# Performance work log

Measured on AMD Instinct MI355X. Metric: run time of the kernel, lower is better.

Reference implementation:

```python
import jax, jax.numpy as jnp
import numpy as np

B, N, S = 64, 128, 100          # batch, pod_num, seq_len
E, H, M = 64, 128, 3            # embed_dim, hidden_dim, modal_num
VOCAB = 2000
FIN = M * S * (E + 1)           # shared_encoder in_features = 19500
FG = M * H                      # gat feature dim = 384
MAX_EVENT_LEN = 100.0
LEAKY_ALPHA = 0.2


def setup_inputs() -> dict:
    key = jax.random.key(0)
    ks = jax.random.split(key, 16)
    inp = {
        "l_e": jax.random.randint(ks[0], (B, N, S), 0, VOCAB),
        "m_e": jax.random.randint(ks[1], (B, N, S), 0, VOCAB),
        "t_e": jax.random.randint(ks[2], (B, N, S), 0, VOCAB),
        "l_c": jax.random.uniform(ks[3], (B, N, S), jnp.float32) * 100.0,
        "m_c": jax.random.uniform(ks[4], (B, N, S), jnp.float32) * 100.0,
        "t_c": jax.random.uniform(ks[5], (B, N, S), jnp.float32) * 100.0,
        "adj": (jax.random.uniform(ks[6], (N, N)) > 0.5).astype(jnp.float32),
        # learned parameters (weights stored as (in, out); y = x @ W + b)
        "emb": jax.random.normal(ks[7], (VOCAB, E), jnp.float32) * 0.02,
        "W_se": jax.random.normal(ks[8], (FIN, 3 * H), jnp.float32) * (1.0 / np.sqrt(FIN)),
        "b_se": jnp.zeros((3 * H,), jnp.float32),
        "gat_W": jax.random.normal(ks[9], (FG, FG), jnp.float32) * (1.0 / np.sqrt(FG)),
        "gat_a": jax.random.normal(ks[10], (2 * FG, 1), jnp.float32) * 0.1,
        "W1": jax.random.normal(ks[11], (FG * N, N), jnp.float32) * (1.0 / np.sqrt(FG * N)),
        "b1": jnp.zeros((N,), jnp.float32),
    }
    return inp


def gat_layer(x, adj, W, a):
    """Faithful GraphAttentionLayer (concat=True, dropout=0) without materializing
    the [B,N,N,2F] a_input: e_ij = leakyrelu(a1.h_i + a2.h_j)."""
    h = x @ W                                      # [B,N,F]
    F_ = W.shape[1]
    a1, a2 = a[:F_, 0], a[F_:, 0]
    e = jax.nn.leaky_relu(
        (h @ a1)[:, :, None] + (h @ a2)[:, None, :], LEAKY_ALPHA
    )                                              # [B,N,N]
    att = jnp.where(adj > 0, e, -1e12)
    att = jax.nn.softmax(att, axis=-1)
    return jax.nn.relu(att @ h)                    # [B,N,F]


def reference(l_e, m_e, t_e, l_c, m_c, t_c, adj, emb, W_se, b_se, gat_W, gat_a, W1, b1):
    # embedding lookup + concat normalized event counts -> [B,N,S,E+1] per modality
    log_r = jnp.concatenate([emb[l_e], (l_c / MAX_EVENT_LEN)[..., None]], -1)
    metric_r = jnp.concatenate([emb[m_e], (m_c / MAX_EVENT_LEN)[..., None]], -1)
    trace_r = jnp.concatenate([emb[t_e], (t_c / MAX_EVENT_LEN)[..., None]], -1)
    # shared encoder: cat on feature dim, flatten per node, dense -> [B,N,3H]
    fused = jnp.concatenate([log_r, metric_r, trace_r], -1).reshape(B, N, -1)
    fusion_r = fused @ W_se + b_se
    # GAT + residual + linear head (use_gat_linear path)
    out = gat_layer(fusion_r, adj, gat_W, gat_a)
    x = fusion_r + out
    x = x.reshape(B, -1) @ W1 + b1                 # [B,N]
    return (x, fusion_r)
```

## Files before the change

kernel.cpp:

```cpp
#include <hip/hip_runtime.h>

#define KB_TOT 305
#define KPAD   19520
#define BROW   39040

typedef __attribute__((ext_vector_type(8))) short bf16x8_t;
typedef __attribute__((ext_vector_type(4))) float f32x4_t;

typedef const __attribute__((address_space(1))) unsigned int GAS_u32;
typedef __attribute__((address_space(3))) unsigned int LAS_u32;

__device__ inline unsigned short f2bf(float x) {
    union { float f; unsigned u; } a; a.f = x;
    unsigned r = a.u + 0x7fffu + ((a.u >> 16) & 1u);
    return (unsigned short)(r >> 16);
}
__device__ inline float bf2f(unsigned short h) {
    union { unsigned u; float f; } a; a.u = ((unsigned)h) << 16; return a.f;
}
__device__ inline unsigned long long pack4bf(float x, float y, float z, float w) {
    return (unsigned long long)f2bf(x) | ((unsigned long long)f2bf(y) << 16)
         | ((unsigned long long)f2bf(z) << 32) | ((unsigned long long)f2bf(w) << 48);
}

__global__ __launch_bounds__(256) void emb_bf_kernel(const float* __restrict__ emb,
                                                     unsigned short* __restrict__ ebf) {
    int i4 = (blockIdx.x * 256 + threadIdx.x) * 4;
    float4 v = *(const float4*)(emb + i4);
    *(unsigned long long*)(ebf + i4) = pack4bf(v.x, v.y, v.z, v.w);
}

__global__ __launch_bounds__(256) void ac_bf_kernel(const float* __restrict__ l_c,
                                                    const float* __restrict__ m_c,
                                                    const float* __restrict__ t_c,
                                                    unsigned short* __restrict__ Ac) {
    int lin = blockIdx.x * 256 + threadIdx.x;
    int row = lin / 80, c4 = (lin - row * 80) * 4;
    float vv[4];
    #pragma unroll
    for (int ii = 0; ii < 4; ++ii) {
        int t = c4 + ii;
        float x = 0.f;
        if (t < 300) {
            int m = t / 100, s = t - m * 100;
            const float* C = (m == 0) ? l_c : ((m == 1) ? m_c : t_c);
            x = C[row * 100 + s] * 0.01f;
        }
        vv[ii] = x;
    }
    *(unsigned long long*)(Ac + row * 320 + c4) = pack4bf(vv[0], vv[1], vv[2], vv[3]);
}

__global__ __launch_bounds__(256) void build_B_kernel(const float* __restrict__ W_se,
                                                      unsigned short* __restrict__ Bws) {
    int kb = blockIdx.x;
    int h0 = blockIdx.y * 64;
    __shared__ float tl[64 * 68];
    int tid = threadIdx.x;
    int rr = tid >> 2, c16 = (tid & 3) * 16;
    float4 v[4];
    if (kb < 300) {
        int m = kb / 100, s = kb - m * 100;
        const float* srcp = W_se + (s * 195 + m * 65 + rr) * 384 + h0 + c16;
        #pragma unroll
        for (int ii = 0; ii < 4; ++ii) v[ii] = *(const float4*)(srcp + ii * 4);
    } else {
        int t = (kb - 300) * 64 + rr;
        if (t < 300) {
            int m = t / 100, s = t - m * 100;
            const float* srcp = W_se + (s * 195 + m * 65 + 64) * 384 + h0 + c16;
            #pragma unroll
            for (int ii = 0; ii < 4; ++ii) v[ii] = *(const float4*)(srcp + ii * 4);
        } else {
            #pragma unroll
            for (int ii = 0; ii < 4; ++ii) v[ii] = make_float4(0.f, 0.f, 0.f, 0.f);
        }
    }
    #pragma unroll
    for (int ii = 0; ii < 4; ++ii) *(float4*)(tl + rr * 68 + c16 + ii * 4) = v[ii];
    __syncthreads();
    int c = tid >> 2, r16 = (tid & 3) * 16;
    unsigned long long* dst8 =
        (unsigned long long*)(Bws + (unsigned)(h0 + c) * KPAD + kb * 64 + r16);
    #pragma unroll
    for (int q = 0; q < 4; ++q) {
        int rb = r16 + q * 4;
        dst8[q] = pack4bf(tl[(rb + 0) * 68 + c], tl[(rb + 1) * 68 + c],
                          tl[(rb + 2) * 68 + c], tl[(rb + 3) * 68 + c]);
    }
}

__global__ __launch_bounds__(256) void wt_bf_kernel(const float* __restrict__ W,
                                                    unsigned short* __restrict__ WT) {
    int k0 = blockIdx.x * 64, n0 = blockIdx.y * 64;
    __shared__ float tl[64 * 68];
    int tid = threadIdx.x;
    int rr = tid >> 2, c16 = (tid & 3) * 16;
    #pragma unroll
    for (int ii = 0; ii < 4; ++ii)
        *(float4*)(tl + rr * 68 + c16 + ii * 4) = *(const float4*)(W + (k0 + rr) * 384 + n0 + c16 + ii * 4);
    __syncthreads();
    int c = tid >> 2, r16 = (tid & 3) * 16;
    unsigned long long* dst8 = (unsigned long long*)(WT + (n0 + c) * 384 + k0 + r16);
    #pragma unroll
    for (int q = 0; q < 4; ++q) {
        int rb = r16 + q * 4;
        dst8[q] = pack4bf(tl[(rb + 0) * 68 + c], tl[(rb + 1) * 68 + c],
                          tl[(rb + 2) * 68 + c], tl[(rb + 3) * 68 + c]);
    }
}

__global__ __launch_bounds__(256) void gemm_fused_kernel(
    const int* __restrict__ l_e, const int* __restrict__ m_e, const int* __restrict__ t_e,
    const unsigned short* __restrict__ emb_bf, const unsigned short* __restrict__ Ac_bf,
    const unsigned short* __restrict__ Bws, float* __restrict__ fusion_d,
    float* __restrict__ P) {

    __shared__ alignas(16) unsigned short Al[128 * 64];
    __shared__ alignas(16) unsigned short Bl[128 * 64];

    const int tid  = threadIdx.x;
    const int lane = tid & 63;
    const int wid  = tid >> 6;

    int bid = blockIdx.x;
    int lin = (bid & 7) * 96 + (bid >> 3);
    const int mt = lin % 64;
    int rest = lin / 64;
    const int nt = rest % 3;
    const int kc = rest / 3;
    const int bm0 = mt * 128;
    const int h0  = nt * 128;
    int kb        = (kc == 0) ? 0 : (77 + (kc - 1) * 76);
    const int kbe = 77 + kc * 76 > KB_TOT ? KB_TOT : 77 + kc * 76;

    const int l7 = lane & 7, l3 = lane >> 3;
    const int voffA = ((l7 ^ l3) << 4);
    const int rowg0 = bm0 + wid * 32 + l3;

    f32x4_t acc[4][4];
    #pragma unroll
    for (int i = 0; i < 4; ++i)
        #pragma unroll
        for (int j = 0; j < 4; ++j) acc[i][j] = (f32x4_t){0.f, 0.f, 0.f, 0.f};

    const int wr = wid >> 1, wc = wid & 1;
    const int l15 = lane & 15, l4 = lane >> 4;

    int idx4[4];
    if (kb < 300) {
        int m = kb / 100, s = kb - m * 100;
        const int* I = (m == 0) ? l_e : ((m == 1) ? m_e : t_e);
        const int* Ib = I + rowg0 * 100 + s;
        idx4[0] = Ib[0]; idx4[1] = Ib[800]; idx4[2] = Ib[1600]; idx4[3] = Ib[2400];
    }

    for (; kb < kbe; ++kb) {
        if (kb < 300) {
            #pragma unroll
            for (int p = 0; p < 4; ++p) {
                const char* src = (const char*)emb_bf + ((long)idx4[p] << 7) + voffA;
                __builtin_amdgcn_global_load_lds((GAS_u32*)src,
                    (LAS_u32*)((char*)Al + (wid * 4 + p) * 1024), 16, 0, 0);
            }
        } else {
            int q = kb - 300;
            #pragma unroll
            for (int p = 0; p < 4; ++p) {
                const char* src = (const char*)Ac_bf + (long)(rowg0 + p * 8) * 640
                                + q * 128 + voffA;
                __builtin_amdgcn_global_load_lds((GAS_u32*)src,
                    (LAS_u32*)((char*)Al + (wid * 4 + p) * 1024), 16, 0, 0);
            }
        }
        #pragma unroll
        for (int p = 0; p < 4; ++p) {
            int ch = wid * 4 + p;
            int hl = ch * 8 + l3;
            long gb = (long)(h0 + hl) * BROW + kb * 128 + ((l7 << 4) ^ (l3 << 4));
            __builtin_amdgcn_global_load_lds((GAS_u32*)((const char*)Bws + gb),
                                             (LAS_u32*)((char*)Bl + ch * 1024), 16, 0, 0);
        }
        int kn = kb + 1;
        if (kn < 300 && kn < kbe) {
            int m = kn / 100, s = kn - m * 100;
            const int* I = (m == 0) ? l_e : ((m == 1) ? m_e : t_e);
            const int* Ib = I + rowg0 * 100 + s;
            idx4[0] = Ib[0]; idx4[1] = Ib[800]; idx4[2] = Ib[1600]; idx4[3] = Ib[2400];
        }
        __syncthreads();
        #pragma unroll
        for (int ks = 0; ks < 2; ++ks) {
            int kb2 = ks * 64 + l4 * 16;
            bf16x8_t af[4], bfr[4];
            #pragma unroll
            for (int i = 0; i < 4; ++i) {
                int row = wr * 64 + i * 16 + l15;
                af[i]  = *(const bf16x8_t*)((const char*)Al + row * 128 + (kb2 ^ ((row & 7) << 4)));
                int col = wc * 64 + i * 16 + l15;
                bfr[i] = *(const bf16x8_t*)((const char*)Bl + col * 128 + (kb2 ^ ((col & 7) << 4)));
            }
            #pragma unroll
            for (int i = 0; i < 4; ++i)
                #pragma unroll
                for (int j = 0; j < 4; ++j)
                    acc[i][j] = __builtin_amdgcn_mfma_f32_16x16x32_bf16(af[i], bfr[j], acc[i][j], 0, 0, 0);
        }
        __syncthreads();
    }
    float* dst = (kc == 0) ? fusion_d : (P + (size_t)(kc - 1) * 3145728);
    #pragma unroll
    for (int i = 0; i < 4; ++i)
        #pragma unroll
        for (int j = 0; j < 4; ++j)
            #pragma unroll
            for (int r = 0; r < 4; ++r) {
                int row = bm0 + wr * 64 + i * 16 + l4 * 4 + r;
                int col = h0 + wc * 64 + j * 16 + l15;
                dst[row * 384 + col] = acc[i][j][r];
            }
}

__global__ __launch_bounds__(256) void reduce_fusion_kernel(float* __restrict__ fusion_d,
                                                            const float* __restrict__ P,
                                                            const float* __restrict__ b_se,
                                                            unsigned short* __restrict__ fusion_bf) {
    int i4 = blockIdx.x * 256 + threadIdx.x;
    int col4 = (i4 % 96) * 4;
    float4 a = *(const float4*)(fusion_d + i4 * 4);
    float4 p0 = *(const float4*)(P + (size_t)i4 * 4);
    float4 p1 = *(const float4*)(P + 3145728 + (size_t)i4 * 4);
    float4 p2 = *(const float4*)(P + 6291456 + (size_t)i4 * 4);
    float4 bs = *(const float4*)(b_se + col4);
    float4 r;
    r.x = a.x + p0.x + p1.x + p2.x + bs.x;
    r.y = a.y + p0.y + p1.y + p2.y + bs.y;
    r.z = a.z + p0.z + p1.z + p2.z + bs.z;
    r.w = a.w + p0.w + p1.w + p2.w + bs.w;
    *(float4*)(fusion_d + i4 * 4) = r;
    *(unsigned long long*)(fusion_bf + i4 * 4) = pack4bf(r.x, r.y, r.z, r.w);
}

__global__ __launch_bounds__(256) void gat_h_kernel(const unsigned short* __restrict__ fusion_bf,
                                                    const unsigned short* __restrict__ WT,
                                                    unsigned short* __restrict__ hT) {
    __shared__ alignas(16) unsigned short Al[128 * 64];
    __shared__ alignas(16) unsigned short Bl[128 * 64];
    const int tid  = threadIdx.x;
    const int lane = tid & 63;
    const int wid  = tid >> 6;
    const int b  = blockIdx.x;
    const int c0 = blockIdx.y * 128;
    const int l7 = lane & 7, l3 = lane >> 3;
    const int voffA = ((l7 ^ l3) << 4);
    const int wr = wid >> 1, wc = wid & 1;
    const int l15 = lane & 15, l4 = lane >> 4;

    f32x4_t acc[4][4];
    #pragma unroll
    for (int i = 0; i < 4; ++i)
        #pragma unroll
        for (int j = 0; j < 4; ++j) acc[i][j] = (f32x4_t){0.f, 0.f, 0.f, 0.f};

    for (int kb = 0; kb < 6; ++kb) {
        #pragma unroll
        for (int p = 0; p < 4; ++p) {
            int ch = wid * 4 + p;
            int rl = ch * 8 + l3;
            long ga = (long)(b * 128 + rl) * 768 + kb * 128 + voffA;
            __builtin_amdgcn_global_load_lds((GAS_u32*)((const char*)fusion_bf + ga),
                                             (LAS_u32*)((char*)Al + ch * 1024), 16, 0, 0);
            long gb = (long)(c0 + rl) * 768 + kb * 128 + voffA;
            __builtin_amdgcn_global_load_lds((GAS_u32*)((const char*)WT + gb),
                                             (LAS_u32*)((char*)Bl + ch * 1024), 16, 0, 0);
        }
        __syncthreads();
        #pragma unroll
        for (int ks = 0; ks < 2; ++ks) {
            int kb2 = ks * 64 + l4 * 16;
            bf16x8_t af[4], bfr[4];
            #pragma unroll
            for (int i = 0; i < 4; ++i) {
                int row = wr * 64 + i * 16 + l15;
                af[i]  = *(const bf16x8_t*)((const char*)Al + row * 128 + (kb2 ^ ((row & 7) << 4)));
                int col = wc * 64 + i * 16 + l15;
                bfr[i] = *(const bf16x8_t*)((const char*)Bl + col * 128 + (kb2 ^ ((col & 7) << 4)));
            }
            #pragma unroll
            for (int i = 0; i < 4; ++i)
                #pragma unroll
                for (int j = 0; j < 4; ++j)
                    acc[i][j] = __builtin_amdgcn_mfma_f32_16x16x32_bf16(af[i], bfr[j], acc[i][j], 0, 0, 0);
        }
        __syncthreads();
    }
    #pragma unroll
    for (int i = 0; i < 4; ++i)
        #pragma unroll
        for (int j = 0; j < 4; ++j) {
            int nb = wr * 64 + i * 16 + l4 * 4;
            int f  = c0 + wc * 64 + j * 16 + l15;
            *(unsigned long long*)(hT + ((size_t)(b * 384 + f)) * 128 + nb) =
                pack4bf(acc[i][j][0], acc[i][j][1], acc[i][j][2], acc[i][j][3]);
        }
}

__global__ __launch_bounds__(256) void gat_att_kernel(const unsigned short* __restrict__ hT,
                                                      const float* __restrict__ gat_a,
                                                      const float* __restrict__ adj,
                                                      unsigned short* __restrict__ att_bf) {
    int b = blockIdx.x;
    __shared__ float e1[128], e2[128];
    __shared__ float av[768];
    int tid = threadIdx.x;
    av[tid] = gat_a[tid];
    av[tid + 256] = gat_a[tid + 256];
    av[tid + 512] = gat_a[tid + 512];
    __syncthreads();
    {
        int n = tid & 127, which = tid >> 7;
        const unsigned short* hp = hT + (size_t)b * 49152 + n;
        const float* aw = av + which * 384;
        float acc = 0.f;
        #pragma unroll 8
        for (int f = 0; f < 384; ++f) acc += bf2f(hp[f * 128]) * aw[f];
        if (which) e2[n] = acc; else e1[n] = acc;
    }
    __syncthreads();
    int r = tid >> 1, half = tid & 1;
    const float* arow = adj + r * 128 + half * 64;
    const float* e2h = e2 + half * 64;
    float er = e1[r];
    float mx = -1e30f;
    #pragma unroll 8
    for (int j = 0; j < 64; ++j) {
        float v = er + e2h[j];
        v = (v > 0.f) ? v : 0.2f * v;
        v = (arow[j] > 0.f) ? v : -1e12f;
        mx = fmaxf(mx, v);
    }
    mx = fmaxf(mx, __shfl_xor(mx, 1));
    float sum = 0.f;
    #pragma unroll 8
    for (int j = 0; j < 64; ++j) {
        float v = er + e2h[j];
        v = (v > 0.f) ? v : 0.2f * v;
        v = (arow[j] > 0.f) ? v : -1e12f;
        sum += __expf(v - mx);
    }
    sum += __shfl_xor(sum, 1);
    float inv = 1.f / sum;
    unsigned short* orow = att_bf + (size_t)b * 16384 + r * 128 + half * 64;
    #pragma unroll 8
    for (int j = 0; j < 64; ++j) {
        float v = er + e2h[j];
        v = (v > 0.f) ? v : 0.2f * v;
        v = (arow[j] > 0.f) ? v : -1e12f;
        orow[j] = f2bf(__expf(v - mx) * inv);
    }
}

__global__ __launch_bounds__(256) void gat_pv_kernel(const unsigned short* __restrict__ att_bf,
                                                     const unsigned short* __restrict__ hT,
                                                     const float* __restrict__ fusion_d,
                                                     unsigned short* __restrict__ x_pre_bf) {
    __shared__ alignas(16) unsigned short Al[128 * 64];
    __shared__ alignas(16) unsigned short Bl[128 * 64];
    const int tid  = threadIdx.x;
    const int lane = tid & 63;
    const int wid  = tid >> 6;
    const int b  = blockIdx.x;
    const int f0 = blockIdx.y * 128;
    const int l7 = lane & 7, l3 = lane >> 3;
    const int voffA = ((l7 ^ l3) << 4);
    const int wr = wid >> 1, wc = wid & 1;
    const int l15 = lane & 15, l4 = lane >> 4;

    f32x4_t acc[4][4];
    #pragma unroll
    for (int i = 0; i < 4; ++i)
        #pragma unroll
        for (int j = 0; j < 4; ++j) acc[i][j] = (f32x4_t){0.f, 0.f, 0.f, 0.f};

    for (int kb = 0; kb < 2; ++kb) {
        #pragma unroll
        for (int p = 0; p < 4; ++p) {
            int ch = wid * 4 + p;
            int rl = ch * 8 + l3;
            long ga = (long)b * 32768 + (long)rl * 256 + kb * 128 + voffA;
            __builtin_amdgcn_global_load_lds((GAS_u32*)((const char*)att_bf + ga),
                                             (LAS_u32*)((char*)Al + ch * 1024), 16, 0, 0);
            long gb = (long)(b * 384 + f0 + rl) * 256 + kb * 128 + voffA;
            __builtin_amdgcn_global_load_lds((GAS_u32*)((const char*)hT + gb),
                                             (LAS_u32*)((char*)Bl + ch * 1024), 16, 0, 0);
        }
        __syncthreads();
        #pragma unroll
        for (int ks = 0; ks < 2; ++ks) {
            int kb2 = ks * 64 + l4 * 16;
            bf16x8_t af[4], bfr[4];
            #pragma unroll
            for (int i = 0; i < 4; ++i) {
                int row = wr * 64 + i * 16 + l15;
                af[i]  = *(const bf16x8_t*)((const char*)Al + row * 128 + (kb2 ^ ((row & 7) << 4)));
                int col = wc * 64 + i * 16 + l15;
                bfr[i] = *(const bf16x8_t*)((const char*)Bl + col * 128 + (kb2 ^ ((col & 7) << 4)));
            }
            #pragma unroll
            for (int i = 0; i < 4; ++i)
                #pragma unroll
                for (int j = 0; j < 4; ++j)
                    acc[i][j] = __builtin_amdgcn_mfma_f32_16x16x32_bf16(af[i], bfr[j], acc[i][j], 0, 0, 0);
        }
        __syncthreads();
    }
    #pragma unroll
    for (int i = 0; i < 4; ++i)
        #pragma unroll
        for (int j = 0; j < 4; ++j) {
            int f = f0 + wc * 64 + j * 16 + l15;
            #pragma unroll
            for (int r = 0; r < 4; ++r) {
                int n = wr * 64 + i * 16 + l4 * 4 + r;
                float v = acc[i][j][r];
                v = (v > 0.f ? v : 0.f) + fusion_d[(b * 128 + n) * 384 + f];
                x_pre_bf[(size_t)b * 49152 + n * 384 + f] = f2bf(v);
            }
        }
}

__global__ __launch_bounds__(256) void final_kernel(const unsigned short* __restrict__ x_pre_bf,
                                                    const float* __restrict__ W1,
                                                    float* __restrict__ pf) {
    int n = blockIdx.x;
    int q = blockIdx.y;
    __shared__ float xl[64 * 196];
    int tid = threadIdx.x;
    #pragma unroll
    for (int p = 0; p < 6; ++p) {
        int e = p * 2048 + tid * 8;
        int b = e / 192, f = e - b * 192;
        bf16x8_t v8 = *(const bf16x8_t*)(x_pre_bf + (size_t)b * 49152 + n * 384 + q * 192 + f);
        float* d = xl + b * 196 + f;
        #pragma unroll
        for (int ii = 0; ii < 8; ++ii) d[ii] = bf2f((unsigned short)v8[ii]);
    }
    __syncthreads();
    int col = (tid & 31) * 4, bh = tid >> 5;
    float acc[8][4] = {};
    #pragma unroll 2
    for (int f = 0; f < 192; ++f) {
        float4 w = *(const float4*)(W1 + ((size_t)(n * 384 + q * 192 + f)) * 128 + col);
        #pragma unroll
        for (int bb = 0; bb < 8; ++bb) {
            float xv = xl[(bh * 8 + bb) * 196 + f];
            acc[bb][0] += xv * w.x; acc[bb][1] += xv * w.y;
            acc[bb][2] += xv * w.z; acc[bb][3] += xv * w.w;
        }
    }
    int slot = n * 2 + q;
    #pragma unroll
    for (int bb = 0; bb < 8; ++bb) {
        int b = bh * 8 + bb;
        *(float4*)(pf + (size_t)slot * 8192 + b * 128 + col) =
            make_float4(acc[bb][0], acc[bb][1], acc[bb][2], acc[bb][3]);
    }
}

__global__ __launch_bounds__(256) void reduce_final_kernel(const float* __restrict__ pf,
                                                           const float* __restrict__ b1,
                                                           float* __restrict__ xout) {
    int i = blockIdx.x * 256 + threadIdx.x;
    float acc = 0.f;
    for (int s = 0; s < 256; ++s) acc += pf[(size_t)s * 8192 + i];
    xout[i] = acc + b1[i & 127];
}

extern "C" void kernel_launch(void* const* d_in, const int* in_sizes, int n_in,
                              void* d_out, int out_size, void* d_ws, size_t ws_size,
                              hipStream_t stream) {
    (void)in_sizes; (void)n_in; (void)out_size; (void)ws_size;
    const int*   l_e   = (const int*)d_in[0];
    const int*   m_e   = (const int*)d_in[1];
    const int*   t_e   = (const int*)d_in[2];
    const float* l_c   = (const float*)d_in[3];
    const float* m_c   = (const float*)d_in[4];
    const float* t_c   = (const float*)d_in[5];
    const float* adj   = (const float*)d_in[6];
    const float* emb   = (const float*)d_in[7];
    const float* W_se  = (const float*)d_in[8];
    const float* b_se  = (const float*)d_in[9];
    const float* gat_W = (const float*)d_in[10];
    const float* gat_a = (const float*)d_in[11];
    const float* W1    = (const float*)d_in[12];
    const float* b1    = (const float*)d_in[13];

    float* xout     = (float*)d_out;
    float* fusion_d = xout + 8192;

    char* ws = (char*)d_ws;
    unsigned short* Bws    = (unsigned short*)(ws);
    unsigned short* emb_bf = (unsigned short*)(ws + 15728640);
    unsigned short* Ac_bf  = (unsigned short*)(ws + 15990784);
    unsigned short* WT_bf  = (unsigned short*)(ws + 21233664);
    float*          P      = (float*)(ws + 21528576);
    unsigned short* fusion_bf = (unsigned short*)(ws);
    unsigned short* hT_bf     = (unsigned short*)(ws + 6291456);
    unsigned short* att_bf    = (unsigned short*)(ws + 12582912);
    unsigned short* x_pre_bf  = (unsigned short*)(ws + 14680064);
    float*          pf        = (float*)(ws + 21528576);

    emb_bf_kernel<<<125, 256, 0, stream>>>(emb, emb_bf);
    ac_bf_kernel<<<2560, 256, 0, stream>>>(l_c, m_c, t_c, Ac_bf);
    build_B_kernel<<<dim3(305, 6), 256, 0, stream>>>(W_se, Bws);
    wt_bf_kernel<<<dim3(6, 6), 256, 0, stream>>>(gat_W, WT_bf);
    gemm_fused_kernel<<<768, 256, 0, stream>>>(l_e, m_e, t_e, emb_bf, Ac_bf, Bws, fusion_d, P);
    reduce_fusion_kernel<<<3072, 256, 0, stream>>>(fusion_d, P, b_se, fusion_bf);
    gat_h_kernel<<<dim3(64, 3), 256, 0, stream>>>(fusion_bf, WT_bf, hT_bf);
    gat_att_kernel<<<64, 256, 0, stream>>>(hT_bf, gat_a, adj, att_bf);
    gat_pv_kernel<<<dim3(64, 3), 256, 0, stream>>>(att_bf, hT_bf, fusion_d, x_pre_bf);
    final_kernel<<<dim3(128, 2), 256, 0, stream>>>(x_pre_bf, W1, pf);
    reduce_final_kernel<<<32, 256, 0, stream>>>(pf, b1, xout);
}
```

Baseline: 379.1 us.

## Fuse prep kernels and fold GAT attention into h and PV kernels

Merges the four preprocessing kernels into one launch that dispatches on block index. Computes the attention logits e1/e2 inside the GAT h GEMM epilogue, using a wave reduction followed by atomicAdd into a buffer that the reduce kernel zeroes. Moves the softmax into the PV kernel, which writes the probabilities straight to LDS and runs the whole K=128 in one stage, removing the att kernel and its global round trip. The cost is atomics, higher LDS use (64KB per block), and softmax work repeated across the three f-blocks.

```diff
diff --git a/kernel.cpp b/kernel.cpp
--- a/kernel.cpp
+++ b/kernel.cpp
@@ -23,90 +23,85 @@
          | ((unsigned long long)f2bf(z) << 32) | ((unsigned long long)f2bf(w) << 48);
 }
 
-__global__ __launch_bounds__(256) void emb_bf_kernel(const float* __restrict__ emb,
-                                                     unsigned short* __restrict__ ebf) {
-    int i4 = (blockIdx.x * 256 + threadIdx.x) * 4;
-    float4 v = *(const float4*)(emb + i4);
-    *(unsigned long long*)(ebf + i4) = pack4bf(v.x, v.y, v.z, v.w);
-}
-
-__global__ __launch_bounds__(256) void ac_bf_kernel(const float* __restrict__ l_c,
-                                                    const float* __restrict__ m_c,
-                                                    const float* __restrict__ t_c,
-                                                    unsigned short* __restrict__ Ac) {
-    int lin = blockIdx.x * 256 + threadIdx.x;
-    int row = lin / 80, c4 = (lin - row * 80) * 4;
-    float vv[4];
-    #pragma unroll
-    for (int ii = 0; ii < 4; ++ii) {
-        int t = c4 + ii;
-        float x = 0.f;
-        if (t < 300) {
-            int m = t / 100, s = t - m * 100;
-            const float* C = (m == 0) ? l_c : ((m == 1) ? m_c : t_c);
-            x = C[row * 100 + s] * 0.01f;
-        }
-        vv[ii] = x;
-    }
-    *(unsigned long long*)(Ac + row * 320 + c4) = pack4bf(vv[0], vv[1], vv[2], vv[3]);
-}
-
-__global__ __launch_bounds__(256) void build_B_kernel(const float* __restrict__ W_se,
-                                                      unsigned short* __restrict__ Bws) {
-    int kb = blockIdx.x;
-    int h0 = blockIdx.y * 64;
+__global__ __launch_bounds__(256) void prep_kernel(
+    const float* __restrict__ emb, const float* __restrict__ l_c,
+    const float* __restrict__ m_c, const float* __restrict__ t_c,
+    const float* __restrict__ W_se, const float* __restrict__ gat_W,
+    unsigned short* __restrict__ ebf, unsigned short* __restrict__ Ac,
+    unsigned short* __restrict__ WT, unsigned short* __restrict__ Bws) {
     __shared__ float tl[64 * 68];
-    int tid = threadIdx.x;
-    int rr = tid >> 2, c16 = (tid & 3) * 16;
-    float4 v[4];
-    if (kb < 300) {
-        int m = kb / 100, s = kb - m * 100;
-        const float* srcp = W_se + (s * 195 + m * 65 + rr) * 384 + h0 + c16;
-        #pragma unroll
-        for (int ii = 0; ii < 4; ++ii) v[ii] = *(const float4*)(srcp + ii * 4);
+    int bid = blockIdx.x, tid = threadIdx.x;
+    if (bid < 125) {
+        int i4 = (bid * 256 + tid) * 4;
+        float4 v = *(const float4*)(emb + i4);
+        *(unsigned long long*)(ebf + i4) = pack4bf(v.x, v.y, v.z, v.w);
+    } else if (bid < 2685) {
+        int lin = (bid - 125) * 256 + tid;
+        int row = lin / 80, c4 = (lin - row * 80) * 4;
+        float vv[4];
+        #pragma unroll
+        for (int ii = 0; ii < 4; ++ii) {
+            int t = c4 + ii;
+            float x = 0.f;
+            if (t < 300) {
+                int m = t / 100, s = t - m * 100;
+                const float* C = (m == 0) ? l_c : ((m == 1) ? m_c : t_c);
+                x = C[row * 100 + s] * 0.01f;
+            }
+            vv[ii] = x;
+        }
+        *(unsigned long long*)(Ac + row * 320 + c4) = pack4bf(vv[0], vv[1], vv[2], vv[3]);
+    } else if (bid < 2721) {
+        int idx = bid - 2685;
+        int k0 = (idx % 6) * 64, n0 = (idx / 6) * 64;
+        int rr = tid >> 2, c16 = (tid & 3) * 16;
+        #pragma unroll
+        for (int ii = 0; ii < 4; ++ii)
+            *(float4*)(tl + rr * 68 + c16 + ii * 4) =
+                *(const float4*)(gat_W + (k0 + rr) * 384 + n0 + c16 + ii * 4);
+        __syncthreads();
+        int c = tid >> 2, r16 = (tid & 3) * 16;
+        unsigned long long* dst8 = (unsigned long long*)(WT + (n0 + c) * 384 + k0 + r16);
+        #pragma unroll
+        for (int q = 0; q < 4; ++q) {
+            int rb = r16 + q * 4;
+            dst8[q] = pack4bf(tl[(rb + 0) * 68 + c], tl[(rb + 1) * 68 + c],
+                              tl[(rb + 2) * 68 + c], tl[(rb + 3) * 68 + c]);
+        }
     } else {
-        int t = (kb - 300) * 64 + rr;
-        if (t < 300) {
-            int m = t / 100, s = t - m * 100;
-            const float* srcp = W_se + (s * 195 + m * 65 + 64) * 384 + h0 + c16;
+        int idx = bid - 2721;
+        int kb = idx % 305, h0 = (idx / 305) * 64;
+        int rr = tid >> 2, c16 = (tid & 3) * 16;
+        float4 v[4];
+        if (kb < 300) {
+            int m = kb / 100, s = kb - m * 100;
+            const float* srcp = W_se + (s * 195 + m * 65 + rr) * 384 + h0 + c16;
             #pragma unroll
             for (int ii = 0; ii < 4; ++ii) v[ii] = *(const float4*)(srcp + ii * 4);
         } else {
-            #pragma unroll
-            for (int ii = 0; ii < 4; ++ii) v[ii] = make_float4(0.f, 0.f, 0.f, 0.f);
-        }
-    }
-    #pragma unroll
-    for (int ii = 0; ii < 4; ++ii) *(float4*)(tl + rr * 68 + c16 + ii * 4) = v[ii];
-    __syncthreads();
-    int c = tid >> 2, r16 = (tid & 3) * 16;
-    unsigned long long* dst8 =
-        (unsigned long long*)(Bws + (unsigned)(h0 + c) * KPAD + kb * 64 + r16);
-    #pragma unroll
-    for (int q = 0; q < 4; ++q) {
-        int rb = r16 + q * 4;
-        dst8[q] = pack4bf(tl[(rb + 0) * 68 + c], tl[(rb + 1) * 68 + c],
-                          tl[(rb + 2) * 68 + c], tl[(rb + 3) * 68 + c]);
-    }
-}
-
-__global__ __launch_bounds__(256) void wt_bf_kernel(const float* __restrict__ W,
-                                                    unsigned short* __restrict__ WT) {
-    int k0 = blockIdx.x * 64, n0 = blockIdx.y * 64;
-    __shared__ float tl[64 * 68];
-    int tid = threadIdx.x;
-    int rr = tid >> 2, c16 = (tid & 3) * 16;
-    #pragma unroll
-    for (int ii = 0; ii < 4; ++ii)
-        *(float4*)(tl + rr * 68 + c16 + ii * 4) = *(const float4*)(W + (k0 + rr) * 384 + n0 + c16 + ii * 4);
-    __syncthreads();
-    int c = tid >> 2, r16 = (tid & 3) * 16;
-    unsigned long long* dst8 = (unsigned long long*)(WT + (n0 + c) * 384 + k0 + r16);
-    #pragma unroll
-    for (int q = 0; q < 4; ++q) {
-        int rb = r16 + q * 4;
-        dst8[q] = pack4bf(tl[(rb + 0) * 68 + c], tl[(rb + 1) * 68 + c],
-                          tl[(rb + 2) * 68 + c], tl[(rb + 3) * 68 + c]);
+            int t = (kb - 300) * 64 + rr;
+            if (t < 300) {
+                int m = t / 100, s = t - m * 100;
+                const float* srcp = W_se + (s * 195 + m * 65 + 64) * 384 + h0 + c16;
+                #pragma unroll
+                for (int ii = 0; ii < 4; ++ii) v[ii] = *(const float4*)(srcp + ii * 4);
+            } else {
+                #pragma unroll
+                for (int ii = 0; ii < 4; ++ii) v[ii] = make_float4(0.f, 0.f, 0.f, 0.f);
+            }
+        }
+        #pragma unroll
+        for (int ii = 0; ii < 4; ++ii) *(float4*)(tl + rr * 68 + c16 + ii * 4) = v[ii];
+        __syncthreads();
+        int c = tid >> 2, r16 = (tid & 3) * 16;
+        unsigned long long* dst8 =
+            (unsigned long long*)(Bws + (unsigned)(h0 + c) * KPAD + kb * 64 + r16);
+        #pragma unroll
+        for (int q = 0; q < 4; ++q) {
+            int rb = r16 + q * 4;
+            dst8[q] = pack4bf(tl[(rb + 0) * 68 + c], tl[(rb + 1) * 68 + c],
+                              tl[(rb + 2) * 68 + c], tl[(rb + 3) * 68 + c]);
+        }
     }
 }
 
@@ -224,7 +219,12 @@
 __global__ __launch_bounds__(256) void reduce_fusion_kernel(float* __restrict__ fusion_d,
                                                             const float* __restrict__ P,
                                                             const float* __restrict__ b_se,
-                                                            unsigned short* __restrict__ fusion_bf) {
+                                                            unsigned short* __restrict__ fusion_bf,
+                                                            float* __restrict__ e_ws) {
+    if (blockIdx.x < 16) {
+        int z = blockIdx.x * 1024 + threadIdx.x * 4;
+        *(float4*)(e_ws + z) = make_float4(0.f, 0.f, 0.f, 0.f);
+    }
     int i4 = blockIdx.x * 256 + threadIdx.x;
     int col4 = (i4 % 96) * 4;
     float4 a = *(const float4*)(fusion_d + i4 * 4);
@@ -243,7 +243,9 @@
 
 __global__ __launch_bounds__(256) void gat_h_kernel(const unsigned short* __restrict__ fusion_bf,
                                                     const unsigned short* __restrict__ WT,
-                                                    unsigned short* __restrict__ hT) {
+                                                    const float* __restrict__ gat_a,
+                                                    unsigned short* __restrict__ hT,
+                                                    float* __restrict__ e_ws) {
     __shared__ alignas(16) unsigned short Al[128 * 64];
     __shared__ alignas(16) unsigned short Bl[128 * 64];
     const int tid  = threadIdx.x;
@@ -303,116 +305,128 @@
             *(unsigned long long*)(hT + ((size_t)(b * 384 + f)) * 128 + nb) =
                 pack4bf(acc[i][j][0], acc[i][j][1], acc[i][j][2], acc[i][j][3]);
         }
-}
-
-__global__ __launch_bounds__(256) void gat_att_kernel(const unsigned short* __restrict__ hT,
-                                                      const float* __restrict__ gat_a,
-                                                      const float* __restrict__ adj,
-                                                      unsigned short* __restrict__ att_bf) {
-    int b = blockIdx.x;
-    __shared__ float e1[128], e2[128];
-    __shared__ float av[768];
-    int tid = threadIdx.x;
-    av[tid] = gat_a[tid];
-    av[tid + 256] = gat_a[tid + 256];
-    av[tid + 512] = gat_a[tid + 512];
-    __syncthreads();
-    {
-        int n = tid & 127, which = tid >> 7;
-        const unsigned short* hp = hT + (size_t)b * 49152 + n;
-        const float* aw = av + which * 384;
-        float acc = 0.f;
-        #pragma unroll 8
-        for (int f = 0; f < 384; ++f) acc += bf2f(hp[f * 128]) * aw[f];
-        if (which) e2[n] = acc; else e1[n] = acc;
-    }
-    __syncthreads();
-    int r = tid >> 1, half = tid & 1;
-    const float* arow = adj + r * 128 + half * 64;
-    const float* e2h = e2 + half * 64;
-    float er = e1[r];
-    float mx = -1e30f;
-    #pragma unroll 8
-    for (int j = 0; j < 64; ++j) {
-        float v = er + e2h[j];
-        v = (v > 0.f) ? v : 0.2f * v;
-        v = (arow[j] > 0.f) ? v : -1e12f;
-        mx = fmaxf(mx, v);
-    }
-    mx = fmaxf(mx, __shfl_xor(mx, 1));
-    float sum = 0.f;
-    #pragma unroll 8
-    for (int j = 0; j < 64; ++j) {
-        float v = er + e2h[j];
-        v = (v > 0.f) ? v : 0.2f * v;
-        v = (arow[j] > 0.f) ? v : -1e12f;
-        sum += __expf(v - mx);
-    }
-    sum += __shfl_xor(sum, 1);
-    float inv = 1.f / sum;
-    unsigned short* orow = att_bf + (size_t)b * 16384 + r * 128 + half * 64;
-    #pragma unroll 8
-    for (int j = 0; j < 64; ++j) {
-        float v = er + e2h[j];
-        v = (v > 0.f) ? v : 0.2f * v;
-        v = (arow[j] > 0.f) ? v : -1e12f;
-        orow[j] = f2bf(__expf(v - mx) * inv);
-    }
-}
-
-__global__ __launch_bounds__(256) void gat_pv_kernel(const unsigned short* __restrict__ att_bf,
+    float a1v[4], a2v[4];
+    #pragma unroll
+    for (int j = 0; j < 4; ++j) {
+        int f = c0 + wc * 64 + j * 16 + l15;
+        a1v[j] = gat_a[f];
+        a2v[j] = gat_a[384 + f];
+    }
+    #pragma unroll
+    for (int i = 0; i < 4; ++i)
+        #pragma unroll
+        for (int r = 0; r < 4; ++r) {
+            float p1 = 0.f, p2 = 0.f;
+            #pragma unroll
+            for (int j = 0; j < 4; ++j) {
+                float hv = acc[i][j][r];
+                p1 += hv * a1v[j];
+                p2 += hv * a2v[j];
+            }
+            #pragma unroll
+            for (int m = 1; m < 16; m <<= 1) {
+                p1 += __shfl_xor(p1, m);
+                p2 += __shfl_xor(p2, m);
+            }
+            if (l15 == 0) {
+                int n = wr * 64 + i * 16 + l4 * 4 + r;
+                atomicAdd(&e_ws[b * 128 + n], p1);
+                atomicAdd(&e_ws[8192 + b * 128 + n], p2);
+            }
+        }
+}
+
+__global__ __launch_bounds__(256) void gat_pv_kernel(const float* __restrict__ e_ws,
+                                                     const float* __restrict__ adj,
                                                      const unsigned short* __restrict__ hT,
                                                      const float* __restrict__ fusion_d,
                                                      unsigned short* __restrict__ x_pre_bf) {
-    __shared__ alignas(16) unsigned short Al[128 * 64];
-    __shared__ alignas(16) unsigned short Bl[128 * 64];
+    __shared__ alignas(16) unsigned short Pl[128 * 128];
+    __shared__ alignas(16) unsigned short Bl[128 * 128];
+    __shared__ float se2[128];
     const int tid  = threadIdx.x;
     const int lane = tid & 63;
     const int wid  = tid >> 6;
     const int b  = blockIdx.x;
     const int f0 = blockIdx.y * 128;
-    const int l7 = lane & 7, l3 = lane >> 3;
-    const int voffA = ((l7 ^ l3) << 4);
     const int wr = wid >> 1, wc = wid & 1;
     const int l15 = lane & 15, l4 = lane >> 4;
 
+    if (tid < 128) se2[tid] = e_ws[8192 + b * 128 + tid];
+    #pragma unroll
+    for (int p = 0; p < 8; ++p) {
+        int ch = wid * 8 + p;
+        int row = ch * 4 + (lane >> 4);
+        long gb = (long)(b * 384 + f0 + row) * 256 + (((lane & 15) ^ (row & 7)) << 4);
+        __builtin_amdgcn_global_load_lds((GAS_u32*)((const char*)hT + gb),
+                                         (LAS_u32*)((char*)Bl + ch * 1024), 16, 0, 0);
+    }
+    __syncthreads();
+
+    {
+        int r = tid >> 1, half = tid & 1;
+        float er = e_ws[b * 128 + r];
+        const float* arow = adj + r * 128 + half * 64;
+        const float* e2h = se2 + half * 64;
+        float mx = -1e30f;
+        #pragma unroll 8
+        for (int j = 0; j < 64; ++j) {
+            float v = er + e2h[j];
+            v = (v > 0.f) ? v : 0.2f * v;
+            v = (arow[j] > 0.f) ? v : -1e12f;
+            mx = fmaxf(mx, v);
+        }
+        mx = fmaxf(mx, __shfl_xor(mx, 1));
+        float sum = 0.f;
+        #pragma unroll 8
+        for (int j = 0; j < 64; ++j) {
+            float v = er + e2h[j];
+            v = (v > 0.f) ? v : 0.2f * v;
+            v = (arow[j] > 0.f) ? v : -1e12f;
+            sum += __expf(v - mx);
+        }
+        sum += __shfl_xor(sum, 1);
+        float inv = 1.f / sum;
+        #pragma unroll
+        for (int g = 0; g < 8; ++g) {
+            float vv[8];
+            #pragma unroll
+            for (int q = 0; q < 8; ++q) {
+                int j = g * 8 + q;
+                float v = er + e2h[j];
+                v = (v > 0.f) ? v : 0.2f * v;
+                v = (arow[j] > 0.f) ? v : -1e12f;
+                vv[q] = __expf(v - mx) * inv;
+            }
+            char* dst = (char*)Pl + r * 256 + ((half * 128 + g * 16) ^ ((r & 7) << 4));
+            *(unsigned long long*)dst       = pack4bf(vv[0], vv[1], vv[2], vv[3]);
+            *(unsigned long long*)(dst + 8) = pack4bf(vv[4], vv[5], vv[6], vv[7]);
+        }
+    }
+    __syncthreads();
+
     f32x4_t acc[4][4];
     #pragma unroll
     for (int i = 0; i < 4; ++i)
         #pragma unroll
         for (int j = 0; j < 4; ++j) acc[i][j] = (f32x4_t){0.f, 0.f, 0.f, 0.f};
 
-    for (int kb = 0; kb < 2; ++kb) {
-        #pragma unroll
-        for (int p = 0; p < 4; ++p) {
-            int ch = wid * 4 + p;
-            int rl = ch * 8 + l3;
-            long ga = (long)b * 32768 + (long)rl * 256 + kb * 128 + voffA;
-            __builtin_amdgcn_global_load_lds((GAS_u32*)((const char*)att_bf + ga),
-                                             (LAS_u32*)((char*)Al + ch * 1024), 16, 0, 0);
-            long gb = (long)(b * 384 + f0 + rl) * 256 + kb * 128 + voffA;
-            __builtin_amdgcn_global_load_lds((GAS_u32*)((const char*)hT + gb),
-                                             (LAS_u32*)((char*)Bl + ch * 1024), 16, 0, 0);
-        }
-        __syncthreads();
-        #pragma unroll
-        for (int ks = 0; ks < 2; ++ks) {
-            int kb2 = ks * 64 + l4 * 16;
-            bf16x8_t af[4], bfr[4];
-            #pragma unroll
-            for (int i = 0; i < 4; ++i) {
-                int row = wr * 64 + i * 16 + l15;
-                af[i]  = *(const bf16x8_t*)((const char*)Al + row * 128 + (kb2 ^ ((row & 7) << 4)));
-                int col = wc * 64 + i * 16 + l15;
-                bfr[i] = *(const bf16x8_t*)((const char*)Bl + col * 128 + (kb2 ^ ((col & 7) << 4)));
-            }
-            #pragma unroll
-            for (int i = 0; i < 4; ++i)
-                #pragma unroll
-                for (int j = 0; j < 4; ++j)
-                    acc[i][j] = __builtin_amdgcn_mfma_f32_16x16x32_bf16(af[i], bfr[j], acc[i][j], 0, 0, 0);
-        }
-        __syncthreads();
+    #pragma unroll
+    for (int st = 0; st < 4; ++st) {
+        int ko = st * 64 + l4 * 16;
+        bf16x8_t af[4], bfr[4];
+        #pragma unroll
+        for (int i = 0; i < 4; ++i) {
+            int row = wr * 64 + i * 16 + l15;
+            af[i]  = *(const bf16x8_t*)((const char*)Pl + row * 256 + (ko ^ ((row & 7) << 4)));
+            int col = wc * 64 + i * 16 + l15;
+            bfr[i] = *(const bf16x8_t*)((const char*)Bl + col * 256 + (ko ^ ((col & 7) << 4)));
+        }
+        #pragma unroll
+        for (int i = 0; i < 4; ++i)
+            #pragma unroll
+            for (int j = 0; j < 4; ++j)
+                acc[i][j] = __builtin_amdgcn_mfma_f32_16x16x32_bf16(af[i], bfr[j], acc[i][j], 0, 0, 0);
     }
     #pragma unroll
     for (int i = 0; i < 4; ++i)
@@ -506,19 +520,16 @@
     float*          P      = (float*)(ws + 21528576);
     unsigned short* fusion_bf = (unsigned short*)(ws);
     unsigned short* hT_bf     = (unsigned short*)(ws + 6291456);
-    unsigned short* att_bf    = (unsigned short*)(ws + 12582912);
-    unsigned short* x_pre_bf  = (unsigned short*)(ws + 14680064);
+    unsigned short* x_pre_bf  = (unsigned short*)(ws + 12582912);
+    float*          e_ws      = (float*)(ws + 18874368);
     float*          pf        = (float*)(ws + 21528576);
 
-    emb_bf_kernel<<<125, 256, 0, stream>>>(emb, emb_bf);
-    ac_bf_kernel<<<2560, 256, 0, stream>>>(l_c, m_c, t_c, Ac_bf);
-    build_B_kernel<<<dim3(305, 6), 256, 0, stream>>>(W_se, Bws);
-    wt_bf_kernel<<<dim3(6, 6), 256, 0, stream>>>(gat_W, WT_bf);
+    prep_kernel<<<4551, 256, 0, stream>>>(emb, l_c, m_c, t_c, W_se, gat_W,
+                                          emb_bf, Ac_bf, WT_bf, Bws);
     gemm_fused_kernel<<<768, 256, 0, stream>>>(l_e, m_e, t_e, emb_bf, Ac_bf, Bws, fusion_d, P);
-    reduce_fusion_kernel<<<3072, 256, 0, stream>>>(fusion_d, P, b_se, fusion_bf);
-    gat_h_kernel<<<dim3(64, 3), 256, 0, stream>>>(fusion_bf, WT_bf, hT_bf);
-    gat_att_kernel<<<64, 256, 0, stream>>>(hT_bf, gat_a, adj, att_bf);
-    gat_pv_kernel<<<dim3(64, 3), 256, 0, stream>>>(att_bf, hT_bf, fusion_d, x_pre_bf);
+    reduce_fusion_kernel<<<3072, 256, 0, stream>>>(fusion_d, P, b_se, fusion_bf, e_ws);
+    gat_h_kernel<<<dim3(64, 3), 256, 0, stream>>>(fusion_bf, WT_bf, gat_a, hT_bf, e_ws);
+    gat_pv_kernel<<<dim3(64, 3), 256, 0, stream>>>(e_ws, adj, hT_bf, fusion_d, x_pre_bf);
     final_kernel<<<dim3(128, 2), 256, 0, stream>>>(x_pre_bf, W1, pf);
     reduce_final_kernel<<<32, 256, 0, stream>>>(pf, b1, xout);
 }
```

Result: faster. 360.6 us (-4.9%).
